# Optimization experiments

Measured on AMD Instinct MI355X. Metric: run time of the kernel, lower is better.

## Reference

```python
import jax, jax.numpy as jnp
import numpy as np

K = 3  # inferred kernel size (28->26->pool->13->11->pool->5 matches 32*5*5 FC input)


def _patches(x, k=K):
    # x: (N,C,H,W) -> (N,C,k*k,OH,OW) valid patches, stride 1
    N, C, H, W = x.shape
    OH, OW = H - k + 1, W - k + 1
    return jnp.stack(
        [x[:, :, i:i + OH, j:j + OW] for i in range(k) for j in range(k)], axis=2
    )


def _maxpool2(x):
    N, C, H, W = x.shape
    H2, W2 = H // 2, W // 2
    x = x[:, :, :H2 * 2, :W2 * 2].reshape(N, C, H2, 2, W2, 2)
    return x.max(axis=(3, 5))


def _lc2d(x, w, b):
    # unshared-weight locally connected conv: w (O,C,k*k,OH,OW), b (O,OH,OW)
    p = _patches(x)  # (N,C,k*k,OH,OW)
    return jnp.einsum('nckij,ockij->noij', p, w) + b


def setup_inputs():
    key = jax.random.key(0)
    ks = jax.random.split(key, 9)
    s = 0.05
    return {
        'x': jax.random.normal(ks[0], (4096, 1, 28, 28), jnp.float32),
        'w1': jax.random.normal(ks[1], (16, 1, 9, 26, 26), jnp.float32) * s,
        'b1': jax.random.normal(ks[2], (16, 26, 26), jnp.float32) * s,
        'w2': jax.random.normal(ks[3], (32, 16, 9, 11, 11), jnp.float32) * s,
        'b2': jax.random.normal(ks[4], (32, 11, 11), jnp.float32) * s,
        'fc1_w': jax.random.normal(ks[5], (32 * 5 * 5, 128), jnp.float32) * s,
        'fc1_b': jax.random.normal(ks[6], (128,), jnp.float32) * s,
        'fc2_w': jax.random.normal(ks[7], (128, 10), jnp.float32) * s,
        'fc2_b': jax.random.normal(ks[8], (10,), jnp.float32) * s,
    }


def reference(x, w1, b1, w2, b2, fc1_w, fc1_b, fc2_w, fc2_b):
    h = _maxpool2(jax.nn.relu(_lc2d(x, w1, b1)))      # (N,16,13,13)
    h = _maxpool2(jax.nn.relu(_lc2d(h, w2, b2)))      # (N,32,5,5)
    h = h.reshape(h.shape[0], -1)                      # (N,800)
    h = jax.nn.relu(h @ fc1_w + fc1_b)                 # (N,128)
    return h @ fc2_w + fc2_b                           # (N,10)
```

## Files before the change

### kernel.cpp

```cpp
#include <hip/hip_runtime.h>

#define NB 4096

typedef __attribute__((ext_vector_type(8))) short s8v;
typedef __attribute__((ext_vector_type(4))) float f4v;

#define XB_OFF  0u
#define H1B_OFF 6422528u
#define H2B_OFF 28573696u
#define W2B_OFF 35127296u
#define B2R_OFF 36765696u
#define W1B_OFF 36778496u
#define B1R_OFF 37470720u
#define WFB_OFF 37513984u

__device__ __forceinline__ unsigned short f2bf(float f) {
  unsigned int u = __builtin_bit_cast(unsigned int, f);
  u += 0x7fffu + ((u >> 16) & 1u);
  return (unsigned short)(u >> 16);
}

__global__ __launch_bounds__(256) void k_prep(const float* __restrict__ x,
                                              const float* __restrict__ w1,
                                              const float* __restrict__ b1,
                                              const float* __restrict__ w2,
                                              const float* __restrict__ b2,
                                              const float* __restrict__ f1w,
                                              short* __restrict__ xB,
                                              short* __restrict__ w1b,
                                              float* __restrict__ b1r,
                                              short* __restrict__ w2b,
                                              float* __restrict__ b2r,
                                              short* __restrict__ wfb) {
  const int bx = blockIdx.x;
  if (bx < 1600) {
    __shared__ float t2[64][33];
    const int c0 = (bx % 25) * 32;
    const int n0 = (bx / 25) * 64;
    const int tx = threadIdx.x & 31, ty = threadIdx.x >> 5;
    const int c = c0 + tx;
    #pragma unroll
    for (int i = 0; i < 64; i += 8)
      if (c < 784) t2[ty + i][tx] = x[(n0 + ty + i) * 784 + c];
    __syncthreads();
    const int cl = threadIdx.x >> 3;
    const int ns = (threadIdx.x & 7) * 8;
    if (c0 + cl < 784) {
      unsigned short v[8];
      #pragma unroll
      for (int q = 0; q < 8; q++) v[q] = f2bf(t2[ns + q][cl]);
      *reinterpret_cast<s8v*>(&xB[(c0 + cl) * NB + n0 + ns]) =
          *reinterpret_cast<const s8v*>(v);
    }
  } else if (bx < 2952) {
    const int idx = (bx - 1600) * 256 + threadIdx.x;
    const int t = idx & 7;
    const int l = (idx >> 3) & 63;
    const int cv = (idx >> 9) & 3;
    const int pos = idx >> 11;
    const int k = (l >> 4) * 8 + t;
    const int o = l & 15;
    const int i = pos / 13, j = pos % 13;
    const int dy = cv >> 1, dx = cv & 1;
    float v = 0.f;
    if (k < 16) {
      const int py = k >> 2, px = k & 3;
      const int ky = py - dy, kx = px - dx;
      if (ky >= 0 && ky < 3 && kx >= 0 && kx < 3)
        v = w1[(o * 9 + ky * 3 + kx) * 676 + (2 * i + dy) * 26 + 2 * j + dx];
    }
    w1b[idx] = (short)f2bf(v);
  } else if (bx < 2995) {
    const int idx = (bx - 2952) * 256 + threadIdx.x;
    if (idx < 10816) {
      const int cv = idx & 3;
      const int o = (idx >> 2) & 15;
      const int pos = idx >> 6;
      const int i = pos / 13, j = pos % 13;
      b1r[idx] = b1[(o * 26 + 2 * i + (cv >> 1)) * 26 + 2 * j + (cv & 1)];
    }
  } else if (bx < 6195) {
    const int idx = (bx - 2995) * 256 + threadIdx.x;
    const int t = idx & 7;
    const int l = (idx >> 3) & 63;
    const int ot = (idx >> 9) & 1;
    const int s = (idx >> 10) & 7;
    const int cv = (idx >> 13) & 3;
    const int pos = idx >> 15;
    const int k = s * 32 + (l >> 4) * 8 + t;
    const int o = ot * 16 + (l & 15);
    const int w = k >> 4, c = k & 15;
    const int py = w >> 2, px = w & 3;
    const int dy = cv >> 1, dx = cv & 1;
    const int ky = py - dy, kx = px - dx;
    const int I = pos / 5, J = pos % 5;
    float v = 0.f;
    if (ky >= 0 && ky < 3 && kx >= 0 && kx < 3)
      v = w2[((o * 16 + c) * 9 + ky * 3 + kx) * 121 +
             (2 * I + dy) * 11 + (2 * J + dx)];
    w2b[idx] = (short)f2bf(v);
  } else if (bx == 6195) {
    for (int q = threadIdx.x; q < 3200; q += 256) {
      const int pos = q >> 7;
      const int r = q & 127;
      const int o = r >> 2, cv = r & 3;
      const int I = pos / 5, J = pos % 5;
      b2r[q] = b2[o * 121 + (2 * I + (cv >> 1)) * 11 + 2 * J + (cv & 1)];
    }
  } else {
    const int idx = (bx - 6196) * 256 + threadIdx.x;
    const int t = idx & 7;
    const int l = (idx >> 3) & 63;
    const int jt = (idx >> 9) & 7;
    const int s = idx >> 12;
    const int o = (l >> 4) * 8 + t;
    const int j = jt * 16 + (l & 15);
    wfb[idx] = (short)f2bf(f1w[(o * 25 + s) * 128 + j]);
  }
}

__global__ __launch_bounds__(256, 3) void k_lc1(const short* __restrict__ xB,
                                                const short* __restrict__ w1b,
                                                const float* __restrict__ b1r,
                                                short* __restrict__ h1b) {
  __shared__ short sx[16 * 264 + 16 + 8];
  __shared__ unsigned short ush[256 * 24];
  const int pos = blockIdx.y;
  const int i = pos / 13, j = pos % 13;
  const int tid = threadIdx.x;
  const int l = tid & 63;
  const int wv = tid >> 6;
  const int lm = l & 15, kg = l >> 4;
  const int n0b = blockIdx.x * 256;

  #pragma unroll
  for (int rr = 0; rr < 2; rr++) {
    const int idx = rr * 256 + tid;
    const int row = idx >> 5, seg = idx & 31;
    const int grow = (2 * i + (row >> 2)) * 28 + (2 * j + (row & 3));
    *reinterpret_cast<s8v*>(&sx[row * 264 + ((row >> 3) & 1) * 16 + seg * 8]) =
        *reinterpret_cast<const s8v*>(&xB[grow * NB + n0b + seg * 8]);
  }

  s8v bf[4];
  #pragma unroll
  for (int cv = 0; cv < 4; cv++)
    bf[cv] = *reinterpret_cast<const s8v*>(w1b + ((pos * 4 + cv) * 64 + l) * 8);
  const float4 bias = *reinterpret_cast<const float4*>(b1r + (pos * 16 + lm) * 4);
  __syncthreads();

  f4v acc[4][4];
  #pragma unroll
  for (int a = 0; a < 4; a++)
    #pragma unroll
    for (int cv = 0; cv < 4; cv++) acc[a][cv] = (f4v){0.f, 0.f, 0.f, 0.f};

  #pragma unroll
  for (int a = 0; a < 4; a++) {
    const int nl = wv * 64 + a * 16 + lm;
    s8v av = (s8v){0, 0, 0, 0, 0, 0, 0, 0};
    if (kg < 2) {
      #pragma unroll
      for (int t = 0; t < 8; t++) {
        const int k = kg * 8 + t;
        av[t] = sx[k * 264 + ((k >> 3) & 1) * 16 + nl];
      }
    }
    #pragma unroll
    for (int cv = 0; cv < 4; cv++)
      acc[a][cv] =
          __builtin_amdgcn_mfma_f32_16x16x32_bf16(av, bf[cv], acc[a][cv], 0, 0, 0);
  }

  #pragma unroll
  for (int a = 0; a < 4; a++) {
    #pragma unroll
    for (int reg = 0; reg < 4; reg++) {
      const int nl = wv * 64 + a * 16 + kg * 4 + reg;
      const float v =
          fmaxf(fmaxf(acc[a][0][reg] + bias.x, acc[a][1][reg] + bias.y),
                fmaxf(acc[a][2][reg] + bias.z, acc[a][3][reg] + bias.w));
      ush[nl * 24 + lm] = f2bf(fmaxf(v, 0.f));
    }
  }
  __syncthreads();

  short* dst = h1b + (pos * 4096 + n0b + tid) * 16;
  const unsigned short* src = ush + tid * 24;
  *reinterpret_cast<s8v*>(dst) = *reinterpret_cast<const s8v*>(src);
  *reinterpret_cast<s8v*>(dst + 8) = *reinterpret_cast<const s8v*>(src + 8);
}

__global__ __launch_bounds__(256, 4) void k_lc2(const short* __restrict__ h1b,
                                                const short* __restrict__ w2b,
                                                const float* __restrict__ b2r,
                                                short* __restrict__ h2b) {
  const int pos = blockIdx.y;
  const int I = pos / 5, J = pos % 5;
  const int tid = threadIdx.x;
  const int l = tid & 63;
  const int wave = tid >> 6;
  const int wm = wave >> 1, ot = wave & 1;
  const int nw = blockIdx.x * 128 + wm * 64;
  const int kg = l >> 4;
  const int lm = l & 15;
  const int c0 = (kg & 1) * 8;
  const int whalf = kg >> 1;

  f4v acc[4][4];
  #pragma unroll
  for (int a = 0; a < 4; a++)
    #pragma unroll
    for (int cv = 0; cv < 4; cv++)
      acc[a][cv] = (f4v){0.f, 0.f, 0.f, 0.f};

  #pragma unroll
  for (int s = 0; s < 8; s++) {
    const int wdw = s * 2 + whalf;
    const int py = wdw >> 2, px = wdw & 3;
    const int p = (2 * I + py) * 13 + (2 * J + px);
    const int abase = (p * 4096 + nw + lm) * 16 + c0;
    s8v av[4];
    #pragma unroll
    for (int a = 0; a < 4; a++)
      av[a] = *reinterpret_cast<const s8v*>(h1b + abase + a * 256);
    #pragma unroll
    for (int cv = 0; cv < 4; cv++) {
      const s8v bf = *reinterpret_cast<const s8v*>(
          w2b + ((((pos * 4 + cv) * 8 + s) * 2 + ot) * 64 + l) * 8);
      #pragma unroll
      for (int a = 0; a < 4; a++)
        acc[a][cv] =
            __builtin_amdgcn_mfma_f32_16x16x32_bf16(av[a], bf, acc[a][cv], 0, 0, 0);
    }
  }

  const int o = ot * 16 + lm;
  const float4 bias = *reinterpret_cast<const float4*>(b2r + (pos * 32 + o) * 4);
  #pragma unroll
  for (int a = 0; a < 4; a++) {
    const int nb = nw + a * 16 + kg * 4;
    #pragma unroll
    for (int reg = 0; reg < 4; reg++) {
      const float v =
          fmaxf(fmaxf(acc[a][0][reg] + bias.x, acc[a][1][reg] + bias.y),
                fmaxf(acc[a][2][reg] + bias.z, acc[a][3][reg] + bias.w));
      h2b[(pos * 4096 + nb + reg) * 32 + o] = (short)f2bf(fmaxf(v, 0.f));
    }
  }
}

__global__ __launch_bounds__(256) void k_fc(const short* __restrict__ h2b,
                                            const short* __restrict__ wfb,
                                            const float* __restrict__ f1b,
                                            const float* __restrict__ f2w,
                                            const float* __restrict__ f2b,
                                            float* __restrict__ out) {
  __shared__ float sh3[128 * 17];
  __shared__ float swf2[128 * 12];
  __shared__ float sb1[128];
  const int tid = threadIdx.x;
  const int l = tid & 63;
  const int w = tid >> 6;
  const int lm = l & 15, kg = l >> 4;
  const int n0 = blockIdx.x * 16;
  const int jt0 = w * 2;

  for (int idx = tid; idx < 1536; idx += 256) {
    const int kk = idx / 12, f = idx % 12;
    swf2[idx] = (f < 10) ? f2w[kk * 10 + f] : 0.f;
  }
  if (tid < 128) sb1[tid] = f1b[tid];

  f4v acc0 = (f4v){0.f, 0.f, 0.f, 0.f};
  f4v acc1 = (f4v){0.f, 0.f, 0.f, 0.f};

  #pragma unroll
  for (int s = 0; s < 25; s++) {
    const s8v av = *reinterpret_cast<const s8v*>(
        h2b + (s * 4096 + n0 + lm) * 32 + kg * 8);
    const s8v b0 = *reinterpret_cast<const s8v*>(
        wfb + ((s * 8 + jt0) * 64 + l) * 8);
    const s8v b1v = *reinterpret_cast<const s8v*>(
        wfb + ((s * 8 + jt0 + 1) * 64 + l) * 8);
    acc0 = __builtin_amdgcn_mfma_f32_16x16x32_bf16(av, b0, acc0, 0, 0, 0);
    acc1 = __builtin_amdgcn_mfma_f32_16x16x32_bf16(av, b1v, acc1, 0, 0, 0);
  }
  __syncthreads();

  #pragma unroll
  for (int q = 0; q < 2; q++) {
    const f4v a = q ? acc1 : acc0;
    const int j = (jt0 + q) * 16 + lm;
    #pragma unroll
    for (int reg = 0; reg < 4; reg++)
      sh3[j * 17 + kg * 4 + reg] = fmaxf(a[reg] + sb1[j], 0.f);
  }
  __syncthreads();

  if (tid < 160) {
    const int oo = tid >> 4, nn = tid & 15;
    float s = f2b[oo];
    for (int j = 0; j < 128; j++)
      s += sh3[j * 17 + nn] * swf2[j * 12 + oo];
    out[(n0 + nn) * 10 + oo] = s;
  }
}

extern "C" void kernel_launch(void* const* d_in, const int* in_sizes, int n_in,
                              void* d_out, int out_size, void* d_ws,
                              size_t ws_size, hipStream_t stream) {
  const float* x   = (const float*)d_in[0];
  const float* w1  = (const float*)d_in[1];
  const float* b1  = (const float*)d_in[2];
  const float* w2  = (const float*)d_in[3];
  const float* b2  = (const float*)d_in[4];
  const float* f1w = (const float*)d_in[5];
  const float* f1b = (const float*)d_in[6];
  const float* f2w = (const float*)d_in[7];
  const float* f2b = (const float*)d_in[8];
  float* out = (float*)d_out;
  char* ws = (char*)d_ws;
  short* xB  = (short*)(ws + XB_OFF);
  short* h1b = (short*)(ws + H1B_OFF);
  short* h2b = (short*)(ws + H2B_OFF);
  short* w2b = (short*)(ws + W2B_OFF);
  float* b2r = (float*)(ws + B2R_OFF);
  short* w1b = (short*)(ws + W1B_OFF);
  float* b1r = (float*)(ws + B1R_OFF);
  short* wfb = (short*)(ws + WFB_OFF);

  k_prep<<<6596, 256, 0, stream>>>(x, w1, b1, w2, b2, f1w,
                                   xB, w1b, b1r, w2b, b2r, wfb);
  k_lc1<<<dim3(16, 169), 256, 0, stream>>>(xB, w1b, b1r, h1b);
  k_lc2<<<dim3(32, 25), 256, 0, stream>>>(h1b, w2b, b2r, h2b);
  k_fc<<<256, 256, 0, stream>>>(h2b, wfb, f1b, f2w, f2b, out);
}
```

Before: 118.2 us.

## Vectorize weight prep writes and stage lc2 weights in shared memory

The prep kernel now has each thread produce eight bf16 weights and write them as one 16-byte store, which cuts the prep grid from 6596 to 2263 blocks. In k_lc2, each block copies its position's 64KB slice of w2b into LDS once, and the MFMA loop then reads B fragments from LDS instead of global memory. To make room for the 64KB of LDS, the launch bound drops to 2 blocks per CU, which lowers occupancy and may expose more latency on the h1b loads.

After: 116.9 us. About the same (-1.1%).

```diff
diff --git a/kernel.cpp b/kernel.cpp
--- a/kernel.cpp
+++ b/kernel.cpp
@@ -52,26 +52,30 @@
       *reinterpret_cast<s8v*>(&xB[(c0 + cl) * NB + n0 + ns]) =
           *reinterpret_cast<const s8v*>(v);
     }
-  } else if (bx < 2952) {
-    const int idx = (bx - 1600) * 256 + threadIdx.x;
-    const int t = idx & 7;
-    const int l = (idx >> 3) & 63;
-    const int cv = (idx >> 9) & 3;
-    const int pos = idx >> 11;
-    const int k = (l >> 4) * 8 + t;
+  } else if (bx < 1769) {
+    const int q = (bx - 1600) * 256 + threadIdx.x;
+    const int l = q & 63;
+    const int cv = (q >> 6) & 3;
+    const int pos = q >> 8;
     const int o = l & 15;
     const int i = pos / 13, j = pos % 13;
     const int dy = cv >> 1, dx = cv & 1;
-    float v = 0.f;
-    if (k < 16) {
-      const int py = k >> 2, px = k & 3;
-      const int ky = py - dy, kx = px - dx;
-      if (ky >= 0 && ky < 3 && kx >= 0 && kx < 3)
-        v = w1[(o * 9 + ky * 3 + kx) * 676 + (2 * i + dy) * 26 + 2 * j + dx];
-    }
-    w1b[idx] = (short)f2bf(v);
-  } else if (bx < 2995) {
-    const int idx = (bx - 2952) * 256 + threadIdx.x;
+    unsigned short v[8];
+    #pragma unroll
+    for (int t = 0; t < 8; t++) {
+      const int k = (l >> 4) * 8 + t;
+      float f = 0.f;
+      if (k < 16) {
+        const int py = k >> 2, px = k & 3;
+        const int ky = py - dy, kx = px - dx;
+        if (ky >= 0 && ky < 3 && kx >= 0 && kx < 3)
+          f = w1[(o * 9 + ky * 3 + kx) * 676 + (2 * i + dy) * 26 + 2 * j + dx];
+      }
+      v[t] = f2bf(f);
+    }
+    *reinterpret_cast<s8v*>(&w1b[q * 8]) = *reinterpret_cast<const s8v*>(v);
+  } else if (bx < 1812) {
+    const int idx = (bx - 1769) * 256 + threadIdx.x;
     if (idx < 10816) {
       const int cv = idx & 3;
       const int o = (idx >> 2) & 15;
@@ -79,27 +83,31 @@
       const int i = pos / 13, j = pos % 13;
       b1r[idx] = b1[(o * 26 + 2 * i + (cv >> 1)) * 26 + 2 * j + (cv & 1)];
     }
-  } else if (bx < 6195) {
-    const int idx = (bx - 2995) * 256 + threadIdx.x;
-    const int t = idx & 7;
-    const int l = (idx >> 3) & 63;
-    const int ot = (idx >> 9) & 1;
-    const int s = (idx >> 10) & 7;
-    const int cv = (idx >> 13) & 3;
-    const int pos = idx >> 15;
-    const int k = s * 32 + (l >> 4) * 8 + t;
+  } else if (bx < 2212) {
+    const int q = (bx - 1812) * 256 + threadIdx.x;
+    const int l = q & 63;
+    const int ot = (q >> 6) & 1;
+    const int s = (q >> 7) & 7;
+    const int cv = (q >> 10) & 3;
+    const int pos = q >> 12;
     const int o = ot * 16 + (l & 15);
-    const int w = k >> 4, c = k & 15;
-    const int py = w >> 2, px = w & 3;
     const int dy = cv >> 1, dx = cv & 1;
-    const int ky = py - dy, kx = px - dx;
     const int I = pos / 5, J = pos % 5;
-    float v = 0.f;
-    if (ky >= 0 && ky < 3 && kx >= 0 && kx < 3)
-      v = w2[((o * 16 + c) * 9 + ky * 3 + kx) * 121 +
-             (2 * I + dy) * 11 + (2 * J + dx)];
-    w2b[idx] = (short)f2bf(v);
-  } else if (bx == 6195) {
+    unsigned short v[8];
+    #pragma unroll
+    for (int t = 0; t < 8; t++) {
+      const int k = s * 32 + (l >> 4) * 8 + t;
+      const int w = k >> 4, c = k & 15;
+      const int py = w >> 2, px = w & 3;
+      const int ky = py - dy, kx = px - dx;
+      float f = 0.f;
+      if (ky >= 0 && ky < 3 && kx >= 0 && kx < 3)
+        f = w2[((o * 16 + c) * 9 + ky * 3 + kx) * 121 +
+               (2 * I + dy) * 11 + (2 * J + dx)];
+      v[t] = f2bf(f);
+    }
+    *reinterpret_cast<s8v*>(&w2b[q * 8]) = *reinterpret_cast<const s8v*>(v);
+  } else if (bx == 2212) {
     for (int q = threadIdx.x; q < 3200; q += 256) {
       const int pos = q >> 7;
       const int r = q & 127;
@@ -108,14 +116,18 @@
       b2r[q] = b2[o * 121 + (2 * I + (cv >> 1)) * 11 + 2 * J + (cv & 1)];
     }
   } else {
-    const int idx = (bx - 6196) * 256 + threadIdx.x;
-    const int t = idx & 7;
-    const int l = (idx >> 3) & 63;
-    const int jt = (idx >> 9) & 7;
-    const int s = idx >> 12;
-    const int o = (l >> 4) * 8 + t;
+    const int q = (bx - 2213) * 256 + threadIdx.x;
+    const int l = q & 63;
+    const int jt = (q >> 6) & 7;
+    const int s = q >> 9;
     const int j = jt * 16 + (l & 15);
-    wfb[idx] = (short)f2bf(f1w[(o * 25 + s) * 128 + j]);
+    unsigned short v[8];
+    #pragma unroll
+    for (int t = 0; t < 8; t++) {
+      const int o = (l >> 4) * 8 + t;
+      v[t] = f2bf(f1w[(o * 25 + s) * 128 + j]);
+    }
+    *reinterpret_cast<s8v*>(&wfb[q * 8]) = *reinterpret_cast<const s8v*>(v);
   }
 }
 
@@ -191,10 +203,11 @@
   *reinterpret_cast<s8v*>(dst + 8) = *reinterpret_cast<const s8v*>(src + 8);
 }
 
-__global__ __launch_bounds__(256, 4) void k_lc2(const short* __restrict__ h1b,
+__global__ __launch_bounds__(256, 2) void k_lc2(const short* __restrict__ h1b,
                                                 const short* __restrict__ w2b,
                                                 const float* __restrict__ b2r,
                                                 short* __restrict__ h2b) {
+  __shared__ short sb[32768];
   const int pos = blockIdx.y;
   const int I = pos / 5, J = pos % 5;
   const int tid = threadIdx.x;
@@ -207,6 +220,15 @@
   const int c0 = (kg & 1) * 8;
   const int whalf = kg >> 1;
 
+  const short* wsrc = w2b + pos * 32768;
+  #pragma unroll
+  for (int r = 0; r < 16; r++) {
+    const int idx = r * 256 + tid;
+    *reinterpret_cast<s8v*>(&sb[idx * 8]) =
+        *reinterpret_cast<const s8v*>(&wsrc[idx * 8]);
+  }
+  __syncthreads();
+
   f4v acc[4][4];
   #pragma unroll
   for (int a = 0; a < 4; a++)
@@ -227,7 +249,7 @@
     #pragma unroll
     for (int cv = 0; cv < 4; cv++) {
       const s8v bf = *reinterpret_cast<const s8v*>(
-          w2b + ((((pos * 4 + cv) * 8 + s) * 2 + ot) * 64 + l) * 8);
+          &sb[(((cv * 8 + s) * 2 + ot) * 64 + l) * 8]);
       #pragma unroll
       for (int a = 0; a < 4; a++)
         acc[a][cv] =
@@ -330,7 +352,7 @@
   float* b1r = (float*)(ws + B1R_OFF);
   short* wfb = (short*)(ws + WFB_OFF);
 
-  k_prep<<<6596, 256, 0, stream>>>(x, w1, b1, w2, b2, f1w,
+  k_prep<<<2263, 256, 0, stream>>>(x, w1, b1, w2, b2, f1w,
                                    xB, w1b, b1r, w2b, b2r, wfb);
   k_lc1<<<dim3(16, 169), 256, 0, stream>>>(xB, w1b, b1r, h1b);
   k_lc2<<<dim3(32, 25), 256, 0, stream>>>(h1b, w2b, b2r, h2b);
```
